# Kernel tuning notes

Measured on AMD Instinct MI355X. Metric: run time of the kernel, lower is better.

Reference implementation:

```python
import jax, jax.numpy as jnp
import numpy as np


def _build_cayley(metric):
    """Cayley table for the Clifford algebra with diagonal metric.
    Blades are indexed by bitmask (0=scalar, 1=e1, 2=e2, 3=e12, 4=e3, ...).
    cayley[i, j, k] = coefficient of blade j in the geometric product e_i * e_k.
    """
    n = len(metric)
    dim = 1 << n
    c = np.zeros((dim, dim, dim), dtype=np.float32)
    for a in range(dim):
        for b in range(dim):
            sign = 1.0
            tmp = a >> 1
            while tmp:  # count basis-vector swaps needed to sort e_a e_b
                if bin(tmp & b).count('1') & 1:
                    sign = -sign
                tmp >>= 1
            common = a & b
            for i in range(n):  # contract repeated basis vectors via the metric
                if common & (1 << i):
                    sign *= metric[i]
            c[a, a ^ b, b] = sign
    return c


def fast_einsum(q_einsum, cayley, k_einsum):
    # geometric product of two multivectors (same einsum as the torch.jit version)
    return jnp.einsum('...i,ijk,...k->...j', q_einsum, cayley, k_einsum)


def _embed_grade1(x, mv_dim):
    # embed a 3D vector as a grade-1 multivector: components at blade bitmasks 1, 2, 4
    mv = jnp.zeros(x.shape[:-1] + (mv_dim,), x.dtype)
    mv = mv.at[..., 1].set(x[..., 0])
    mv = mv.at[..., 2].set(x[..., 1])
    mv = mv.at[..., 4].set(x[..., 2])
    return mv


def setup_inputs() -> dict:
    key = jax.random.key(0)
    k1, k2 = jax.random.split(key)
    B, P, D = 4, 8192, 3
    return {
        'source_cloud': jax.random.normal(k1, (B, P, D), dtype=jnp.float32),
        'target_cloud': jax.random.normal(k2, (B, P, D), dtype=jnp.float32),
        'cayley': jnp.asarray(_build_cayley([1.0, 1.0, 1.0])),  # (8,8,8)
    }


def reference(source_cloud, target_cloud, cayley):
    # KNN (K=1) via full pairwise squared distances: (B, P1, P2)
    d2 = (jnp.sum(source_cloud * source_cloud, -1)[:, :, None]
          + jnp.sum(target_cloud * target_cloud, -1)[:, None, :]
          - 2.0 * jnp.einsum('bid,bjd->bij', source_cloud, target_cloud))
    idx = jnp.argmin(d2, axis=2)  # (B, P1) nearest-neighbor indices (non-differentiable)
    # knn_gather: nn[b, i] = target_cloud[b, idx[b, i]]
    nn = jnp.take_along_axis(target_cloud, idx[..., None], axis=1)  # (B, P1, 3)
    # multivector residual and geometric product with itself via the Cayley table
    diff_mv = _embed_grade1(source_cloud - nn, cayley.shape[0])  # (B, P1, 8)
    gp = fast_einsum(diff_mv, cayley, diff_mv)  # (B, P1, 8)
    # scalar part of v*v equals ||v||^2 under the Euclidean metric
    per_point = gp[..., 0]
    per_cloud = jnp.sum(per_point, axis=1)  # point_reduction='sum'
    return jnp.mean(per_cloud)  # batch_reduction='mean'
```

## Files before the change

kernel.cpp:

```cpp
#include <hip/hip_runtime.h>

#define BATCH 4
#define NPTS 8192
#define NTOT (BATCH * NPTS)

typedef __attribute__((ext_vector_type(8)))  short  short8;
typedef __attribute__((ext_vector_type(16))) float  f32x16;

__device__ __forceinline__ unsigned short f2bf(float f) {
    unsigned u = __float_as_uint(f);
    unsigned r = u + 0x7FFFu + ((u >> 16) & 1u);
    return (unsigned short)(r >> 16);
}
__device__ __forceinline__ float bf2f(unsigned short s) {
    return __uint_as_float(((unsigned)s) << 16);
}

__global__ __launch_bounds__(256) void prep_kernel(
        const float* __restrict__ tgt, short8* __restrict__ packed)
{
    int j = blockIdx.x * 256 + threadIdx.x;
    float x = tgt[3*j+0], y = tgt[3*j+1], z = tgt[3*j+2];
    float n = 0.5f * (x*x + y*y + z*z);
    unsigned short hx = f2bf(x), hy = f2bf(y), hz = f2bf(z), hn = f2bf(n);
    unsigned short lx = f2bf(x - bf2f(hx)), ly = f2bf(y - bf2f(hy)),
                   lz = f2bf(z - bf2f(hz)), ln = f2bf(n - bf2f(hn));
    short8 v = { (short)hx,(short)hy,(short)hz,(short)hn,
                 (short)lx,(short)ly,(short)lz,(short)ln };
    packed[j] = v;
}

__global__ __launch_bounds__(256) void knn_mfma_kernel(
        const float* __restrict__ src, const short8* __restrict__ packed,
        float* __restrict__ slab)
{
    __shared__ short8 tlds[512];

    int gid   = blockIdx.x;
    int half  = gid & 1;
    int chunk = (gid >> 1) & 63;
    int b     = gid >> 7;
    int lane  = threadIdx.x & 63;
    int wave  = threadIdx.x >> 6;
    int col   = lane & 31;
    bool lo   = (lane < 32);

    int p_local = chunk * 128 + wave * 32 + col;

    float sx = 0.f, sy = 0.f, sz = 0.f;
    if (lo) {
        const float* sp = src + ((size_t)b * NPTS + p_local) * 3;
        sx = sp[0]; sy = sp[1]; sz = sp[2];
    }
    float ns2 = sx*sx + sy*sy + sz*sz;

    float nx = -sx, ny = -sy, nz = -sz;
    unsigned short hx = f2bf(nx), hy = f2bf(ny), hz = f2bf(nz);
    unsigned short lx = f2bf(nx - bf2f(hx)), ly = f2bf(ny - bf2f(hy)),
                   lz = f2bf(nz - bf2f(hz));
    const short ONE = (short)0x3F80;
    short8 B1 = {0,0,0,0,0,0,0,0}, B2 = {0,0,0,0,0,0,0,0};
    if (lo) {
        B1 = short8{ (short)hx,(short)hy,(short)hz, ONE,
                     (short)hx,(short)hy,(short)hz, ONE };
        B2 = short8{ (short)lx,(short)ly,(short)lz, 0,
                     (short)lx,(short)ly,(short)lz, 0 };
    }

    const short8* tp = packed + (size_t)b * NPTS + (size_t)half * 4096;

    float mb[8];
    #pragma unroll
    for (int i = 0; i < 8; ++i) mb[i] = INFINITY;

    for (int g = 0; g < 8; ++g) {
        __syncthreads();
        tlds[threadIdx.x]       = tp[g*512 + threadIdx.x];
        tlds[threadIdx.x + 256] = tp[g*512 + 256 + threadIdx.x];
        __syncthreads();
        #pragma unroll 4
        for (int tt = 0; tt < 16; ++tt) {
            short8 A = {0,0,0,0,0,0,0,0};
            if (lo) A = tlds[tt*32 + col];
            f32x16 c = {0,0,0,0,0,0,0,0,0,0,0,0,0,0,0,0};
            c = __builtin_amdgcn_mfma_f32_32x32x16_bf16(A, B1, c, 0, 0, 0);
            c = __builtin_amdgcn_mfma_f32_32x32x16_bf16(A, B2, c, 0, 0, 0);
            #pragma unroll
            for (int i = 0; i < 8; ++i)
                mb[i] = fminf(mb[i], fminf(c[2*i], c[2*i+1]));
        }
    }

    float v = fminf(fminf(fminf(mb[0],mb[1]), fminf(mb[2],mb[3])),
                    fminf(fminf(mb[4],mb[5]), fminf(mb[6],mb[7])));
    v = fminf(v, __shfl_xor(v, 32, 64));
    if (lo)
        slab[(size_t)half * NTOT + (size_t)b * NPTS + p_local] = fmaf(2.0f, v, ns2);
}

__global__ __launch_bounds__(256) void reduce1_kernel(
        const float* __restrict__ slab, float* __restrict__ partials)
{
    __shared__ float acc[256];
    int base = blockIdx.x * 512;
    float a = 0.f;
    #pragma unroll
    for (int p = 0; p < 2; ++p) {
        int i = base + threadIdx.x + p * 256;
        a += fminf(slab[i], slab[NTOT + i]);
    }
    acc[threadIdx.x] = a;
    __syncthreads();
    for (int off = 128; off > 0; off >>= 1) {
        if (threadIdx.x < off) acc[threadIdx.x] += acc[threadIdx.x + off];
        __syncthreads();
    }
    if (threadIdx.x == 0) partials[blockIdx.x] = acc[0];
}

__global__ __launch_bounds__(64) void reduce2_kernel(
        const float* __restrict__ partials, float* __restrict__ out)
{
    float v = partials[threadIdx.x];
    #pragma unroll
    for (int off = 32; off > 0; off >>= 1)
        v += __shfl_down(v, off, 64);
    if (threadIdx.x == 0) out[0] = v * 0.25f;
}

extern "C" void kernel_launch(void* const* d_in, const int* in_sizes, int n_in,
                              void* d_out, int out_size, void* d_ws, size_t ws_size,
                              hipStream_t stream) {
    const float* src = (const float*)d_in[0];
    const float* tgt = (const float*)d_in[1];
    float* out = (float*)d_out;

    short8* packed   = (short8*)d_ws;
    float*  slab     = (float*)((char*)d_ws + (size_t)NTOT * sizeof(short8));
    float*  partials = slab + 2 * NTOT;

    prep_kernel<<<NTOT / 256, 256, 0, stream>>>(tgt, packed);
    knn_mfma_kernel<<<512, 256, 0, stream>>>(src, packed, slab);
    reduce1_kernel<<<64, 256, 0, stream>>>(slab, partials);
    reduce2_kernel<<<1, 64, 0, stream>>>(partials, out);
}
```

Before: 39.62 us.

## Fuse target prep into KNN kernel, merge MFMAs via K-split, fold reductions

The MFMA K dimension is now split across the two half-waves so the hi and lo source parts share one MFMA instead of two, and all 64 lanes carry useful work. Target bf16 hi/lo packing moves inside the KNN kernel, with the next group's loads prefetched into registers. Per-block partial sums are reduced in-kernel, which removes the prep kernel, the slab round-trip and one reduce launch. In exchange the grid halves from 512 to 256 blocks, each block scans all 8192 targets, and the packing work is repeated in every block.

Measured after the change: 50.39 us. 27.2% more time.

```diff
diff --git a/kernel.cpp b/kernel.cpp
--- a/kernel.cpp
+++ b/kernel.cpp
@@ -6,6 +6,9 @@
 
 typedef __attribute__((ext_vector_type(8)))  short  short8;
 typedef __attribute__((ext_vector_type(16))) float  f32x16;
+
+constexpr int GRP  = 512;
+constexpr int NGRP = NPTS / GRP;
 
 __device__ __forceinline__ unsigned short f2bf(float f) {
     unsigned u = __float_as_uint(f);
@@ -16,116 +19,105 @@
     return __uint_as_float(((unsigned)s) << 16);
 }
 
-__global__ __launch_bounds__(256) void prep_kernel(
-        const float* __restrict__ tgt, short8* __restrict__ packed)
+__global__ __launch_bounds__(256) void knn_mfma_kernel(
+        const float* __restrict__ src,
+        const float* __restrict__ tgt,
+        float* __restrict__ partials)
 {
-    int j = blockIdx.x * 256 + threadIdx.x;
-    float x = tgt[3*j+0], y = tgt[3*j+1], z = tgt[3*j+2];
-    float n = 0.5f * (x*x + y*y + z*z);
-    unsigned short hx = f2bf(x), hy = f2bf(y), hz = f2bf(z), hn = f2bf(n);
-    unsigned short lx = f2bf(x - bf2f(hx)), ly = f2bf(y - bf2f(hy)),
-                   lz = f2bf(z - bf2f(hz)), ln = f2bf(n - bf2f(hn));
-    short8 v = { (short)hx,(short)hy,(short)hz,(short)hn,
-                 (short)lx,(short)ly,(short)lz,(short)ln };
-    packed[j] = v;
-}
+    __shared__ short8 tlds[GRP];
+    __shared__ float  wsum[4];
 
-__global__ __launch_bounds__(256) void knn_mfma_kernel(
-        const float* __restrict__ src, const short8* __restrict__ packed,
-        float* __restrict__ slab)
-{
-    __shared__ short8 tlds[512];
-
-    int gid   = blockIdx.x;
-    int half  = gid & 1;
-    int chunk = (gid >> 1) & 63;
-    int b     = gid >> 7;
-    int lane  = threadIdx.x & 63;
-    int wave  = threadIdx.x >> 6;
+    int blk   = blockIdx.x;
+    int b     = blk >> 6;
+    int chunk = blk & 63;
+    int tid   = threadIdx.x;
+    int lane  = tid & 63;
+    int wave  = tid >> 6;
     int col   = lane & 31;
-    bool lo   = (lane < 32);
+    int khalf = lane >> 5;
 
     int p_local = chunk * 128 + wave * 32 + col;
-
-    float sx = 0.f, sy = 0.f, sz = 0.f;
-    if (lo) {
-        const float* sp = src + ((size_t)b * NPTS + p_local) * 3;
-        sx = sp[0]; sy = sp[1]; sz = sp[2];
-    }
-    float ns2 = sx*sx + sy*sy + sz*sz;
+    const float* sp = src + ((size_t)b * NPTS + p_local) * 3;
+    float sx = sp[0], sy = sp[1], sz = sp[2];
+    float ns2 = sx * sx + sy * sy + sz * sz;
 
     float nx = -sx, ny = -sy, nz = -sz;
-    unsigned short hx = f2bf(nx), hy = f2bf(ny), hz = f2bf(nz);
-    unsigned short lx = f2bf(nx - bf2f(hx)), ly = f2bf(ny - bf2f(hy)),
-                   lz = f2bf(nz - bf2f(hz));
+    unsigned short shx = f2bf(nx), shy = f2bf(ny), shz = f2bf(nz);
+    unsigned short slx = f2bf(nx - bf2f(shx)), sly = f2bf(ny - bf2f(shy)),
+                   slz = f2bf(nz - bf2f(shz));
     const short ONE = (short)0x3F80;
-    short8 B1 = {0,0,0,0,0,0,0,0}, B2 = {0,0,0,0,0,0,0,0};
-    if (lo) {
-        B1 = short8{ (short)hx,(short)hy,(short)hz, ONE,
-                     (short)hx,(short)hy,(short)hz, ONE };
-        B2 = short8{ (short)lx,(short)ly,(short)lz, 0,
-                     (short)lx,(short)ly,(short)lz, 0 };
-    }
+    short8 Bf;
+    if (khalf == 0)
+        Bf = short8{ (short)shx,(short)shy,(short)shz, ONE,
+                     (short)shx,(short)shy,(short)shz, ONE };
+    else
+        Bf = short8{ (short)slx,(short)sly,(short)slz, 0, 0,0,0,0 };
 
-    const short8* tp = packed + (size_t)b * NPTS + (size_t)half * 4096;
+    const float2* tbase = (const float2*)(tgt + (size_t)b * NPTS * 3);
+    float2 pa = tbase[tid * 3 + 0], pb = tbase[tid * 3 + 1], pc = tbase[tid * 3 + 2];
 
     float mb[8];
     #pragma unroll
     for (int i = 0; i < 8; ++i) mb[i] = INFINITY;
 
-    for (int g = 0; g < 8; ++g) {
+    for (int g = 0; g < NGRP; ++g) {
+        {
+            float x0 = pa.x, y0 = pa.y, z0 = pb.x;
+            float x1 = pb.y, y1 = pc.x, z1 = pc.y;
+            float n0 = 0.5f * (x0*x0 + y0*y0 + z0*z0);
+            float n1 = 0.5f * (x1*x1 + y1*y1 + z1*z1);
+            unsigned short hx = f2bf(x0), hy = f2bf(y0), hz = f2bf(z0), hn = f2bf(n0);
+            tlds[2*tid] = short8{ (short)hx,(short)hy,(short)hz,(short)hn,
+                                  (short)f2bf(x0 - bf2f(hx)), (short)f2bf(y0 - bf2f(hy)),
+                                  (short)f2bf(z0 - bf2f(hz)), (short)f2bf(n0 - bf2f(hn)) };
+            hx = f2bf(x1); hy = f2bf(y1); hz = f2bf(z1); hn = f2bf(n1);
+            tlds[2*tid+1] = short8{ (short)hx,(short)hy,(short)hz,(short)hn,
+                                    (short)f2bf(x1 - bf2f(hx)), (short)f2bf(y1 - bf2f(hy)),
+                                    (short)f2bf(z1 - bf2f(hz)), (short)f2bf(n1 - bf2f(hn)) };
+        }
+        if (g + 1 < NGRP) {
+            const float2* nb = tbase + (size_t)(g + 1) * (GRP * 3 / 2);
+            pa = nb[tid * 3 + 0]; pb = nb[tid * 3 + 1]; pc = nb[tid * 3 + 2];
+        }
         __syncthreads();
-        tlds[threadIdx.x]       = tp[g*512 + threadIdx.x];
-        tlds[threadIdx.x + 256] = tp[g*512 + 256 + threadIdx.x];
-        __syncthreads();
+
         #pragma unroll 4
-        for (int tt = 0; tt < 16; ++tt) {
-            short8 A = {0,0,0,0,0,0,0,0};
-            if (lo) A = tlds[tt*32 + col];
+        for (int tt = 0; tt < GRP / 32; ++tt) {
+            short8 A = tlds[tt * 32 + col];
             f32x16 c = {0,0,0,0,0,0,0,0,0,0,0,0,0,0,0,0};
-            c = __builtin_amdgcn_mfma_f32_32x32x16_bf16(A, B1, c, 0, 0, 0);
-            c = __builtin_amdgcn_mfma_f32_32x32x16_bf16(A, B2, c, 0, 0, 0);
+            c = __builtin_amdgcn_mfma_f32_32x32x16_bf16(A, Bf, c, 0, 0, 0);
             #pragma unroll
             for (int i = 0; i < 8; ++i)
                 mb[i] = fminf(mb[i], fminf(c[2*i], c[2*i+1]));
         }
+        __syncthreads();
     }
 
-    float v = fminf(fminf(fminf(mb[0],mb[1]), fminf(mb[2],mb[3])),
-                    fminf(fminf(mb[4],mb[5]), fminf(mb[6],mb[7])));
+    float v = fminf(fminf(fminf(mb[0], mb[1]), fminf(mb[2], mb[3])),
+                    fminf(fminf(mb[4], mb[5]), fminf(mb[6], mb[7])));
     v = fminf(v, __shfl_xor(v, 32, 64));
-    if (lo)
-        slab[(size_t)half * NTOT + (size_t)b * NPTS + p_local] = fmaf(2.0f, v, ns2);
+    float d2 = fmaf(2.0f, v, ns2);
+
+    float a = d2;
+    #pragma unroll
+    for (int off = 16; off > 0; off >>= 1)
+        a += __shfl_xor(a, off, 32);
+    if (lane == 0) wsum[wave] = a;
+    __syncthreads();
+    if (tid == 0) partials[blk] = (wsum[0] + wsum[1]) + (wsum[2] + wsum[3]);
 }
 
-__global__ __launch_bounds__(256) void reduce1_kernel(
-        const float* __restrict__ slab, float* __restrict__ partials)
+__global__ __launch_bounds__(256) void reduce_kernel(
+        const float* __restrict__ partials, float* __restrict__ out)
 {
     __shared__ float acc[256];
-    int base = blockIdx.x * 512;
-    float a = 0.f;
-    #pragma unroll
-    for (int p = 0; p < 2; ++p) {
-        int i = base + threadIdx.x + p * 256;
-        a += fminf(slab[i], slab[NTOT + i]);
-    }
-    acc[threadIdx.x] = a;
+    acc[threadIdx.x] = partials[threadIdx.x];
     __syncthreads();
     for (int off = 128; off > 0; off >>= 1) {
         if (threadIdx.x < off) acc[threadIdx.x] += acc[threadIdx.x + off];
         __syncthreads();
     }
-    if (threadIdx.x == 0) partials[blockIdx.x] = acc[0];
-}
-
-__global__ __launch_bounds__(64) void reduce2_kernel(
-        const float* __restrict__ partials, float* __restrict__ out)
-{
-    float v = partials[threadIdx.x];
-    #pragma unroll
-    for (int off = 32; off > 0; off >>= 1)
-        v += __shfl_down(v, off, 64);
-    if (threadIdx.x == 0) out[0] = v * 0.25f;
+    if (threadIdx.x == 0) out[0] = acc[0] * 0.25f;
 }
 
 extern "C" void kernel_launch(void* const* d_in, const int* in_sizes, int n_in,
@@ -133,14 +125,9 @@
                               hipStream_t stream) {
     const float* src = (const float*)d_in[0];
     const float* tgt = (const float*)d_in[1];
-    float* out = (float*)d_out;
+    float* out      = (float*)d_out;
+    float* partials = (float*)d_ws;
 
-    short8* packed   = (short8*)d_ws;
-    float*  slab     = (float*)((char*)d_ws + (size_t)NTOT * sizeof(short8));
-    float*  partials = slab + 2 * NTOT;
-
-    prep_kernel<<<NTOT / 256, 256, 0, stream>>>(tgt, packed);
-    knn_mfma_kernel<<<512, 256, 0, stream>>>(src, packed, slab);
-    reduce1_kernel<<<64, 256, 0, stream>>>(slab, partials);
-    reduce2_kernel<<<1, 64, 0, stream>>>(partials, out);
+    knn_mfma_kernel<<<256, 256, 0, stream>>>(src, tgt, partials);
+    reduce_kernel<<<1, 256, 0, stream>>>(partials, out);
 }
```

## Fold hi/lo bf16 split into one MFMA using both K halves, single-wave blocks

Applied to the files above, without the earlier changes.

Rather than issuing two MFMAs per tile with half of the lanes zeroed, the upper 32 lanes now carry the low-order bf16 correction terms, so a single 32x32x16 MFMA computes the full dot product. The kernel moves to one wave per block with 4096 blocks and splits the target points four ways instead of two. Target tiles are read straight from global memory with a one-tile software prefetch instead of being staged through LDS with barriers, and the reduction takes the min over four slabs. One cross term (source low times target low) is dropped, and the workspace needs twice as many slab entries.

Measured after the change: 35.15 us. 1.13x faster.

```diff
diff --git a/kernel.cpp b/kernel.cpp
--- a/kernel.cpp
+++ b/kernel.cpp
@@ -6,6 +6,10 @@
 
 typedef __attribute__((ext_vector_type(8)))  short  short8;
 typedef __attribute__((ext_vector_type(16))) float  f32x16;
+
+constexpr int NQ    = 4;
+constexpr int QT    = NPTS / NQ;
+constexpr int TILES = QT / 32;
 
 __device__ __forceinline__ unsigned short f2bf(float f) {
     unsigned u = __float_as_uint(f);
@@ -17,85 +21,71 @@
 }
 
 __global__ __launch_bounds__(256) void prep_kernel(
-        const float* __restrict__ tgt, short8* __restrict__ packed)
+        const float* __restrict__ tgt, short8* __restrict__ tq)
 {
     int j = blockIdx.x * 256 + threadIdx.x;
     float x = tgt[3*j+0], y = tgt[3*j+1], z = tgt[3*j+2];
     float n = 0.5f * (x*x + y*y + z*z);
     unsigned short hx = f2bf(x), hy = f2bf(y), hz = f2bf(z), hn = f2bf(n);
-    unsigned short lx = f2bf(x - bf2f(hx)), ly = f2bf(y - bf2f(hy)),
-                   lz = f2bf(z - bf2f(hz)), ln = f2bf(n - bf2f(hn));
-    short8 v = { (short)hx,(short)hy,(short)hz,(short)hn,
-                 (short)lx,(short)ly,(short)lz,(short)ln };
-    packed[j] = v;
+    tq[j] = short8{ (short)hx, (short)hy, (short)hz, (short)hn,
+                    (short)f2bf(x - bf2f(hx)), (short)f2bf(y - bf2f(hy)),
+                    (short)f2bf(z - bf2f(hz)), (short)f2bf(n - bf2f(hn)) };
 }
 
-__global__ __launch_bounds__(256) void knn_mfma_kernel(
-        const float* __restrict__ src, const short8* __restrict__ packed,
+__global__ __launch_bounds__(64) void knn_mfma_kernel(
+        const float* __restrict__ src,
+        const short8* __restrict__ tq,
         float* __restrict__ slab)
 {
-    __shared__ short8 tlds[512];
+    int w     = blockIdx.x;
+    int q     = w & (NQ - 1);
+    int chunk = (w >> 2) & 255;
+    int b     = w >> 10;
+    int lane  = threadIdx.x;
+    int col   = lane & 31;
+    int khalf = lane >> 5;
 
-    int gid   = blockIdx.x;
-    int half  = gid & 1;
-    int chunk = (gid >> 1) & 63;
-    int b     = gid >> 7;
-    int lane  = threadIdx.x & 63;
-    int wave  = threadIdx.x >> 6;
-    int col   = lane & 31;
-    bool lo   = (lane < 32);
-
-    int p_local = chunk * 128 + wave * 32 + col;
-
-    float sx = 0.f, sy = 0.f, sz = 0.f;
-    if (lo) {
-        const float* sp = src + ((size_t)b * NPTS + p_local) * 3;
-        sx = sp[0]; sy = sp[1]; sz = sp[2];
-    }
+    int p_local = chunk * 32 + col;
+    const float* sp = src + ((size_t)b * NPTS + p_local) * 3;
+    float sx = sp[0], sy = sp[1], sz = sp[2];
     float ns2 = sx*sx + sy*sy + sz*sz;
 
     float nx = -sx, ny = -sy, nz = -sz;
-    unsigned short hx = f2bf(nx), hy = f2bf(ny), hz = f2bf(nz);
-    unsigned short lx = f2bf(nx - bf2f(hx)), ly = f2bf(ny - bf2f(hy)),
-                   lz = f2bf(nz - bf2f(hz));
+    unsigned short shx = f2bf(nx), shy = f2bf(ny), shz = f2bf(nz);
+    unsigned short slx = f2bf(nx - bf2f(shx)), sly = f2bf(ny - bf2f(shy)),
+                   slz = f2bf(nz - bf2f(shz));
     const short ONE = (short)0x3F80;
-    short8 B1 = {0,0,0,0,0,0,0,0}, B2 = {0,0,0,0,0,0,0,0};
-    if (lo) {
-        B1 = short8{ (short)hx,(short)hy,(short)hz, ONE,
-                     (short)hx,(short)hy,(short)hz, ONE };
-        B2 = short8{ (short)lx,(short)ly,(short)lz, 0,
-                     (short)lx,(short)ly,(short)lz, 0 };
-    }
+    short8 Bf;
+    if (khalf == 0)
+        Bf = short8{ (short)shx,(short)shy,(short)shz, ONE,
+                     (short)shx,(short)shy,(short)shz, ONE };
+    else
+        Bf = short8{ (short)slx,(short)sly,(short)slz, 0, 0,0,0,0 };
 
-    const short8* tp = packed + (size_t)b * NPTS + (size_t)half * 4096;
+    const short8* tp = tq + (size_t)b * NPTS + (size_t)q * QT;
 
     float mb[8];
     #pragma unroll
     for (int i = 0; i < 8; ++i) mb[i] = INFINITY;
 
-    for (int g = 0; g < 8; ++g) {
-        __syncthreads();
-        tlds[threadIdx.x]       = tp[g*512 + threadIdx.x];
-        tlds[threadIdx.x + 256] = tp[g*512 + 256 + threadIdx.x];
-        __syncthreads();
-        #pragma unroll 4
-        for (int tt = 0; tt < 16; ++tt) {
-            short8 A = {0,0,0,0,0,0,0,0};
-            if (lo) A = tlds[tt*32 + col];
-            f32x16 c = {0,0,0,0,0,0,0,0,0,0,0,0,0,0,0,0};
-            c = __builtin_amdgcn_mfma_f32_32x32x16_bf16(A, B1, c, 0, 0, 0);
-            c = __builtin_amdgcn_mfma_f32_32x32x16_bf16(A, B2, c, 0, 0, 0);
-            #pragma unroll
-            for (int i = 0; i < 8; ++i)
-                mb[i] = fminf(mb[i], fminf(c[2*i], c[2*i+1]));
-        }
+    short8 Anext = tp[col];
+    #pragma unroll 4
+    for (int tt = 0; tt < TILES; ++tt) {
+        short8 A = Anext;
+        if (tt + 1 < TILES) Anext = tp[(tt + 1) * 32 + col];
+        f32x16 c = {0,0,0,0,0,0,0,0,0,0,0,0,0,0,0,0};
+        c = __builtin_amdgcn_mfma_f32_32x32x16_bf16(A, Bf, c, 0, 0, 0);
+        #pragma unroll
+        for (int i = 0; i < 8; ++i)
+            mb[i] = fminf(mb[i], fminf(c[2*i], c[2*i+1]));
     }
 
-    float v = fminf(fminf(fminf(mb[0],mb[1]), fminf(mb[2],mb[3])),
-                    fminf(fminf(mb[4],mb[5]), fminf(mb[6],mb[7])));
+    float v = fminf(fminf(fminf(mb[0], mb[1]), fminf(mb[2], mb[3])),
+                    fminf(fminf(mb[4], mb[5]), fminf(mb[6], mb[7])));
     v = fminf(v, __shfl_xor(v, 32, 64));
-    if (lo)
-        slab[(size_t)half * NTOT + (size_t)b * NPTS + p_local] = fmaf(2.0f, v, ns2);
+    float d2 = fmaf(2.0f, v, ns2);
+    if (lane < 32)
+        slab[(size_t)q * NTOT + (size_t)b * NPTS + p_local] = d2;
 }
 
 __global__ __launch_bounds__(256) void reduce1_kernel(
@@ -103,11 +93,13 @@
 {
     __shared__ float acc[256];
     int base = blockIdx.x * 512;
-    float a = 0.f;
+    float a = 0.0f;
     #pragma unroll
     for (int p = 0; p < 2; ++p) {
         int i = base + threadIdx.x + p * 256;
-        a += fminf(slab[i], slab[NTOT + i]);
+        float m = fminf(fminf(slab[i],            slab[NTOT + i]),
+                        fminf(slab[2*NTOT + i],   slab[3*NTOT + i]));
+        a += m;
     }
     acc[threadIdx.x] = a;
     __syncthreads();
@@ -135,12 +127,12 @@
     const float* tgt = (const float*)d_in[1];
     float* out = (float*)d_out;
 
-    short8* packed   = (short8*)d_ws;
+    short8* tq       = (short8*)d_ws;
     float*  slab     = (float*)((char*)d_ws + (size_t)NTOT * sizeof(short8));
-    float*  partials = slab + 2 * NTOT;
+    float*  partials = slab + (size_t)NQ * NTOT;
 
-    prep_kernel<<<NTOT / 256, 256, 0, stream>>>(tgt, packed);
-    knn_mfma_kernel<<<512, 256, 0, stream>>>(src, packed, slab);
+    prep_kernel<<<NTOT / 256, 256, 0, stream>>>(tgt, tq);
+    knn_mfma_kernel<<<BATCH * 256 * NQ, 64, 0, stream>>>(src, tq, slab);
     reduce1_kernel<<<64, 256, 0, stream>>>(slab, partials);
     reduce2_kernel<<<1, 64, 0, stream>>>(partials, out);
 }
```
